# Optimization experiments

Hardware: AMD Instinct MI355X
Metric: run time of the kernel (lower is better)

## Reference

```python
import jax, jax.numpy as jnp
import numpy as np

E, TOPK, H, I = 8, 2, 2048, 5632
T = 4096


def setup_inputs() -> dict:
    key = jax.random.key(0)
    k1, k2, k3, k4 = jax.random.split(key, 4)
    hidden_states = jax.random.normal(k1, (T, H), dtype=jnp.float32)
    gate_w = jax.random.normal(k2, (E, H), dtype=jnp.float32) * (1.0 / np.sqrt(H))
    # fused gate+up projection: [E, 2*I, H]
    w13 = jax.random.normal(k3, (E, 2 * I, H), dtype=jnp.float32) * (1.0 / np.sqrt(H))
    # down projection: [E, H, I]
    w2 = jax.random.normal(k4, (E, H, I), dtype=jnp.float32) * (1.0 / np.sqrt(I))
    return {"hidden_states": hidden_states, "gate_w": gate_w, "w13": w13, "w2": w2, "top_k": TOPK}


def reference(hidden_states, gate_w, w13, w2, top_k):
    num_experts = gate_w.shape[0]
    inter = w2.shape[2]
    # router: fp32 gate logits -> softmax -> top-k -> renormalize (FusedMoE renormalize=True)
    logits = hidden_states.astype(jnp.float32) @ gate_w.T          # [T, E]
    probs = jax.nn.softmax(logits, axis=-1)
    vals, idx = jax.lax.top_k(probs, top_k)                        # [T, k]
    vals = vals / jnp.sum(vals, axis=-1, keepdims=True)
    # dense routing weight matrix [T, E] (zero outside top-k)
    dense_w = jnp.sum(jax.nn.one_hot(idx, num_experts, dtype=vals.dtype) * vals[..., None], axis=1)

    def body(acc, inputs):
        w13_e, w2_e, we = inputs                                   # [2I,H], [H,I], [T]
        gu = hidden_states @ w13_e.T                               # [T, 2I]
        g, u = gu[:, :inter], gu[:, inter:]
        h = jax.nn.silu(g) * u                                     # SwiGLU
        y = h @ w2_e.T                                             # [T, H]
        return acc + we[:, None] * y, None

    acc0 = jnp.zeros_like(hidden_states)
    out, _ = jax.lax.scan(body, acc0, (w13, w2, dense_w.T))
    return out
```

## Files before the change

kernel.cpp:

```cpp
#include <hip/hip_runtime.h>

#define T_TOK 4096
#define H_DIM 2048
#define I_DIM 5632
#define NE 8

typedef _Float16 f16;
typedef _Float16 f16x8 __attribute__((ext_vector_type(8)));
typedef float f32x4 __attribute__((ext_vector_type(4)));

#define OFF_META   0
#define OFF_BTOK   256
#define OFF_BW     (256 + 32768)
#define OFF_RE     (256 + 2 * 32768)
#define OFF_RW     (256 + 3 * 32768)
#define OFF_TP     (256 + 4 * 32768)
#define OFF_HSB    (256 + 5 * 32768)
#define OFF_WF     (OFF_HSB + (size_t)T_TOK * H_DIM * 2)

typedef const __attribute__((address_space(1))) unsigned int guint;
typedef __attribute__((address_space(3))) unsigned int luint;

__device__ __forceinline__ int swzk(int r, int bir) {
    return (bir & 15) | ((((bir >> 4) ^ r) & 7) << 4);
}

__global__ void cvt_w_kernel(const float* __restrict__ src, f16* __restrict__ dst, int n8) {
    int stride = gridDim.x * blockDim.x;
    for (int i = blockIdx.x * blockDim.x + threadIdx.x; i < n8; i += stride) {
        size_t b = (size_t)i * 8;
        float4 a = *(const float4*)(src + b);
        float4 c = *(const float4*)(src + b + 4);
        f16x8 v;
        v[0] = (f16)a.x; v[1] = (f16)a.y; v[2] = (f16)a.z; v[3] = (f16)a.w;
        v[4] = (f16)c.x; v[5] = (f16)c.y; v[6] = (f16)c.z; v[7] = (f16)c.w;
        *(f16x8*)(dst + b) = v;
    }
}

__global__ void prep_kernel(const float* __restrict__ w13, f16* __restrict__ w13f, int n8_w13,
                            int cvt13_b,
                            const float* __restrict__ hs, f16* __restrict__ hsb,
                            const float* __restrict__ gw,
                            int* __restrict__ re, float* __restrict__ rw,
                            int* __restrict__ counts) {
    int id = blockIdx.x;
    if (id < cvt13_b) {
        int stride = cvt13_b * 256;
        for (int i = id * 256 + threadIdx.x; i < n8_w13; i += stride) {
            size_t b = (size_t)i * 8;
            float4 a = *(const float4*)(w13 + b);
            float4 c = *(const float4*)(w13 + b + 4);
            f16x8 v;
            v[0] = (f16)a.x; v[1] = (f16)a.y; v[2] = (f16)a.z; v[3] = (f16)a.w;
            v[4] = (f16)c.x; v[5] = (f16)c.y; v[6] = (f16)c.z; v[7] = (f16)c.w;
            *(f16x8*)(w13f + b) = v;
        }
        return;
    }
    id -= cvt13_b;
    if (id < 1024) {
        const int n8 = T_TOK * H_DIM / 8;
        int stride = 1024 * 256;
        for (int i = id * 256 + threadIdx.x; i < n8; i += stride) {
            size_t b = (size_t)i * 8;
            float4 a = *(const float4*)(hs + b);
            float4 c = *(const float4*)(hs + b + 4);
            f16x8 v;
            v[0] = (f16)a.x; v[1] = (f16)a.y; v[2] = (f16)a.z; v[3] = (f16)a.w;
            v[4] = (f16)c.x; v[5] = (f16)c.y; v[6] = (f16)c.z; v[7] = (f16)c.w;
            *(f16x8*)(hsb + b) = v;
        }
        return;
    }
    id -= 1024;
    int lane = threadIdx.x & 63;
    int t = id * 4 + (threadIdx.x >> 6);
    float acc[NE];
#pragma unroll
    for (int e = 0; e < NE; ++e) acc[e] = 0.f;
    const float* x = hs + (size_t)t * H_DIM;
    for (int i = lane; i < H_DIM; i += 64) {
        float xv = x[i];
#pragma unroll
        for (int e = 0; e < NE; ++e) acc[e] += xv * gw[e * H_DIM + i];
    }
#pragma unroll
    for (int e = 0; e < NE; ++e)
        for (int off = 32; off > 0; off >>= 1) acc[e] += __shfl_xor(acc[e], off);
    if (lane == 0) {
        int i1 = 0; float l1 = acc[0];
#pragma unroll
        for (int e = 1; e < NE; ++e) if (acc[e] > l1) { l1 = acc[e]; i1 = e; }
        int i2 = -1; float l2 = -1e30f;
#pragma unroll
        for (int e = 0; e < NE; ++e) if (e != i1 && acc[e] > l2) { l2 = acc[e]; i2 = e; }
        float aa = __expf(l2 - l1);
        float s = 1.f / (1.f + aa);
        re[t * 2] = i1; re[t * 2 + 1] = i2;
        rw[t * 2] = s;  rw[t * 2 + 1] = aa * s;
        atomicAdd(&counts[i1], 1);
        atomicAdd(&counts[i2], 1);
    }
}

__global__ void scan_kernel(int* __restrict__ meta) {
    if (threadIdx.x == 0) {
        int s = 0;
        for (int e = 0; e < NE; ++e) { meta[8 + e] = s; meta[16 + e] = s; s += meta[e]; }
    }
}

__global__ void place_kernel(const int* __restrict__ re, const float* __restrict__ rw,
                             int* __restrict__ cursor, int* __restrict__ btok,
                             float* __restrict__ bwv, int* __restrict__ tpos) {
    int t = blockIdx.x * 256 + threadIdx.x;
    if (t >= T_TOK) return;
#pragma unroll
    for (int s = 0; s < 2; ++s) {
        int e = re[t * 2 + s];
        int p = atomicAdd(&cursor[e], 1);
        btok[p] = t;
        bwv[p] = rw[t * 2 + s];
        tpos[t * 2 + s] = p;
    }
}

__device__ __forceinline__ void decode_panel(int id, int npx, int e_arg, int e_base,
                                             int& e, int& bx, int& by) {
    if (e_arg >= 0) { e = e_arg; bx = id >> 5; by = id & 31; return; }
    int sg  = id >> 8;
    int rem = id & 255;
    by = rem >> 3;
    int P = sg * 8 + (rem & 7);
    e = e_base + P / npx; bx = P % npx;
}

__global__ __launch_bounds__(256, 4) void gemm1_kernel(
    const f16* __restrict__ w13f, const f16* __restrict__ hsb, f16* __restrict__ hb,
    const int* __restrict__ counts, const int* __restrict__ offs,
    const int* __restrict__ btok,
    const float* __restrict__ cvt_src, f16* __restrict__ cvt_dst, int cvt_n8, int cvt_blocks,
    int e_arg, int e_base, int global_h)
{
    if ((int)blockIdx.x < cvt_blocks) {
        int stride = cvt_blocks * 256;
        for (int i = blockIdx.x * 256 + threadIdx.x; i < cvt_n8; i += stride) {
            size_t b = (size_t)i * 8;
            float4 a = *(const float4*)(cvt_src + b);
            float4 c = *(const float4*)(cvt_src + b + 4);
            f16x8 v;
            v[0] = (f16)a.x; v[1] = (f16)a.y; v[2] = (f16)a.z; v[3] = (f16)a.w;
            v[4] = (f16)c.x; v[5] = (f16)c.y; v[6] = (f16)c.z; v[7] = (f16)c.w;
            *(f16x8*)(cvt_dst + b) = v;
        }
        return;
    }
    int e, bx, by;
    decode_panel((int)blockIdx.x - cvt_blocks, 88, e_arg, e_base, e, bx, by);
    const int n_e = counts[e];
    if (by * 128 >= n_e) return;
    const int boff = offs[e];
    const f16* We = (e_arg >= 0) ? w13f : (w13f + (size_t)e * (2 * I_DIM) * H_DIM);

    const int tid = threadIdx.x;
    const int lane = tid & 63;
    const int wid = tid >> 6;
    const int wm = wid >> 1, wn = wid & 1;
    const int l15 = lane & 15;

    __shared__ f16 As[128 * 64];
    __shared__ f16 Bs[128 * 64];

    const f16* gA[4]; const f16* gB[4]; int dstc[4];
#pragma unroll
    for (int i = 0; i < 4; ++i) {
        int c = i * 256 + tid;
        int r = c >> 3;
        dstc[i] = c * 16;
        int slot = ((c & 7) ^ (r & 7)) * 8;
        int idx = by * 128 + r;
        idx = idx < n_e ? idx : n_e - 1;
        gA[i] = hsb + (size_t)btok[boff + idx] * H_DIM + slot;
        int wrow = (r < 64) ? (bx * 64 + r) : (I_DIM + bx * 64 + (r - 64));
        gB[i] = We + (size_t)wrow * H_DIM + slot;
    }

    f32x4 ag[4][2], au[4][2];
#pragma unroll
    for (int m = 0; m < 4; ++m)
#pragma unroll
        for (int n = 0; n < 2; ++n) { ag[m][n] = (f32x4)0.f; au[m][n] = (f32x4)0.f; }

    const int NT = H_DIM / 64;

#pragma unroll 1
    for (int kt = 0; kt < NT; ++kt) {
        __syncthreads();
        const int k0 = kt * 64;
#pragma unroll
        for (int i = 0; i < 4; ++i) {
            __builtin_amdgcn_global_load_lds((guint*)(gA[i] + k0), (luint*)((char*)As + dstc[i]), 16, 0, 0);
            __builtin_amdgcn_global_load_lds((guint*)(gB[i] + k0), (luint*)((char*)Bs + dstc[i]), 16, 0, 0);
        }
        __syncthreads();
#pragma unroll
        for (int kh = 0; kh < 2; ++kh) {
            const int kb = kh * 64 + (lane >> 4) * 16;
            f16x8 a[4], bg[2], bu[2];
#pragma unroll
            for (int m = 0; m < 4; ++m) {
                int r = wm * 64 + m * 16 + l15;
                a[m] = *(const f16x8*)((const char*)As + r * 128 + swzk(r, kb));
            }
#pragma unroll
            for (int n = 0; n < 2; ++n) {
                int rg = wn * 32 + n * 16 + l15;
                bg[n] = *(const f16x8*)((const char*)Bs + rg * 128 + swzk(rg, kb));
                int ru = 64 + rg;
                bu[n] = *(const f16x8*)((const char*)Bs + ru * 128 + swzk(ru, kb));
            }
#pragma unroll
            for (int m = 0; m < 4; ++m)
#pragma unroll
                for (int n = 0; n < 2; ++n) {
                    ag[m][n] = __builtin_amdgcn_mfma_f32_16x16x32_f16(a[m], bg[n], ag[m][n], 0, 0, 0);
                    au[m][n] = __builtin_amdgcn_mfma_f32_16x16x32_f16(a[m], bu[n], au[m][n], 0, 0, 0);
                }
        }
    }

    const int hbase = (global_h ? boff : 0) + by * 128;
#pragma unroll
    for (int m = 0; m < 4; ++m) {
        int rl0 = wm * 64 + m * 16 + ((lane >> 4) << 2);
#pragma unroll
        for (int r = 0; r < 4; ++r) {
            int rl = rl0 + r;
            if (by * 128 + rl < n_e) {
#pragma unroll
                for (int n = 0; n < 2; ++n) {
                    float g = ag[m][n][r];
                    float u = au[m][n][r];
                    float h = g / (1.f + __expf(-g)) * u;
                    hb[(size_t)(hbase + rl) * I_DIM + bx * 64 + wn * 32 + n * 16 + l15] = (f16)h;
                }
            }
        }
    }
}

__global__ __launch_bounds__(512, 4) void gemm2_kernel(
    const f16* __restrict__ w2f, const f16* __restrict__ hb, float* __restrict__ y,
    const int* __restrict__ counts, const int* __restrict__ offs,
    const int* __restrict__ btok, int e_arg, int global_h)
{
    int e, bx, by;
    decode_panel(blockIdx.x, 8, e_arg, 0, e, bx, by);
    const int n_e = counts[e];
    if (by * 128 >= n_e) return;
    const int boff = offs[e];
    const f16* We = (e_arg >= 0) ? w2f : (w2f + (size_t)e * H_DIM * I_DIM);

    const int tid = threadIdx.x;
    const int lane = tid & 63;
    const int wid = tid >> 6;
    const int wm = wid >> 2;
    const int wn = wid & 3;
    const int l15 = lane & 15;

    __shared__ f16 As[128 * 64];
    __shared__ f16 Bs[256 * 64];

    const int hb0 = global_h ? boff : 0;
    const f16* gA[2]; int dA[2];
#pragma unroll
    for (int i = 0; i < 2; ++i) {
        int c = i * 512 + tid;
        int r = c >> 3;
        dA[i] = c * 16;
        int slot = ((c & 7) ^ (r & 7)) * 8;
        int idx = by * 128 + r;
        idx = idx < n_e ? idx : n_e - 1;
        gA[i] = hb + (size_t)(hb0 + idx) * I_DIM + slot;
    }
    const f16* gB[4]; int dB[4];
#pragma unroll
    for (int j = 0; j < 4; ++j) {
        int c = j * 512 + tid;
        int r = c >> 3;
        dB[j] = c * 16;
        int slot = ((c & 7) ^ (r & 7)) * 8;
        gB[j] = We + (size_t)(bx * 256 + r) * I_DIM + slot;
    }

    f32x4 acc[4][4];
#pragma unroll
    for (int m = 0; m < 4; ++m)
#pragma unroll
        for (int n = 0; n < 4; ++n) acc[m][n] = (f32x4)0.f;

    const int NT = I_DIM / 64;

#pragma unroll 1
    for (int kt = 0; kt < NT; ++kt) {
        __syncthreads();
        const int k0 = kt * 64;
#pragma unroll
        for (int i = 0; i < 2; ++i)
            __builtin_amdgcn_global_load_lds((guint*)(gA[i] + k0), (luint*)((char*)As + dA[i]), 16, 0, 0);
#pragma unroll
        for (int j = 0; j < 4; ++j)
            __builtin_amdgcn_global_load_lds((guint*)(gB[j] + k0), (luint*)((char*)Bs + dB[j]), 16, 0, 0);
        __syncthreads();
#pragma unroll
        for (int kh = 0; kh < 2; ++kh) {
            const int kb = kh * 64 + (lane >> 4) * 16;
            f16x8 a[4], b[4];
#pragma unroll
            for (int m = 0; m < 4; ++m) {
                int r = wm * 64 + m * 16 + l15;
                a[m] = *(const f16x8*)((const char*)As + r * 128 + swzk(r, kb));
            }
#pragma unroll
            for (int n = 0; n < 4; ++n) {
                int r = wn * 64 + n * 16 + l15;
                b[n] = *(const f16x8*)((const char*)Bs + r * 128 + swzk(r, kb));
            }
#pragma unroll
            for (int m = 0; m < 4; ++m)
#pragma unroll
                for (int n = 0; n < 4; ++n)
                    acc[m][n] = __builtin_amdgcn_mfma_f32_16x16x32_f16(a[m], b[n], acc[m][n], 0, 0, 0);
        }
    }

#pragma unroll
    for (int m = 0; m < 4; ++m) {
        int rl0 = wm * 64 + m * 16 + ((lane >> 4) << 2);
#pragma unroll
        for (int r = 0; r < 4; ++r) {
            int rl = rl0 + r;
            if (by * 128 + rl < n_e) {
                int p = boff + by * 128 + rl;
#pragma unroll
                for (int n = 0; n < 4; ++n)
                    y[(size_t)p * H_DIM + bx * 256 + wn * 64 + n * 16 + l15] = acc[m][n][r];
            }
        }
    }
}

__global__ void reduce_kernel(const float* __restrict__ y, const int* __restrict__ tpos,
                              const float* __restrict__ bwv, float* __restrict__ out) {
    int t = blockIdx.x;
    int p0 = tpos[t * 2], p1 = tpos[t * 2 + 1];
    float w0 = bwv[p0], w1 = bwv[p1];
    const float4* y0 = (const float4*)(y + (size_t)p0 * H_DIM);
    const float4* y1 = (const float4*)(y + (size_t)p1 * H_DIM);
    float4* o = (float4*)(out + (size_t)t * H_DIM);
    for (int i = threadIdx.x; i < H_DIM / 4; i += 256) {
        float4 a = y0[i], b = y1[i];
        float4 r;
        r.x = w0 * a.x + w1 * b.x;
        r.y = w0 * a.y + w1 * b.y;
        r.z = w0 * a.z + w1 * b.z;
        r.w = w0 * a.w + w1 * b.w;
        o[i] = r;
    }
}

extern "C" void kernel_launch(void* const* d_in, const int* in_sizes, int n_in,
                              void* d_out, int out_size, void* d_ws, size_t ws_size,
                              hipStream_t stream) {
    const float* hs  = (const float*)d_in[0];
    const float* gw  = (const float*)d_in[1];
    const float* w13 = (const float*)d_in[2];
    const float* w2  = (const float*)d_in[3];
    float* out = (float*)d_out;

    char* ws = (char*)d_ws;
    int*   meta = (int*)(ws + OFF_META);
    int*   btok = (int*)(ws + OFF_BTOK);
    float* bwv  = (float*)(ws + OFF_BW);
    int*   re   = (int*)(ws + OFF_RE);
    float* rw   = (float*)(ws + OFF_RW);
    int*   tpos = (int*)(ws + OFF_TP);
    f16*   hsb  = (f16*)(ws + OFF_HSB);

    hipMemsetAsync(meta, 0, 256, stream);

    const size_t w13_elems = (size_t)NE * 2 * I_DIM * H_DIM;
    const size_t w13_half  = w13_elems / 2;
    const size_t w2_elems  = (size_t)NE * H_DIM * I_DIM;

    size_t o_w13f = OFF_WF;
    size_t o_w2f  = o_w13f + w13_elems * 2;
    size_t o_hb   = o_w2f + w2_elems * 2;
    size_t o_y    = o_hb + (size_t)2 * T_TOK * I_DIM * 2;
    size_t need_full = o_y + (size_t)2 * T_TOK * H_DIM * 4;

    size_t f_w13 = OFF_WF;
    size_t f_w2  = f_w13 + (size_t)2 * I_DIM * H_DIM * 2;
    size_t f_hb  = f_w2 + (size_t)H_DIM * I_DIM * 2;
    size_t f_y   = f_hb + (size_t)T_TOK * I_DIM * 2;

    if (ws_size >= need_full) {
        f16* w13f = (f16*)(ws + o_w13f);
        f16* w2f  = (f16*)(ws + o_w2f);
        f16* hb   = (f16*)(ws + o_hb);
        float* y  = (float*)(ws + o_y);
        prep_kernel<<<3072 + 1024 + 1024, 256, 0, stream>>>(
            w13, w13f, (int)(w13_half / 8), 3072, hs, hsb, gw, re, rw, meta);
        scan_kernel<<<1, 64, 0, stream>>>(meta);
        place_kernel<<<T_TOK / 256, 256, 0, stream>>>(re, rw, meta + 16, btok, bwv, tpos);
        gemm1_kernel<<<2048 + 352 * 32, 256, 0, stream>>>(
            w13f, hsb, hb, meta, meta + 8, btok,
            w13 + w13_half, (f16*)(ws + o_w13f) + w13_half, (int)(w13_half / 8), 2048, -1, 0, 1);
        gemm1_kernel<<<2048 + 352 * 32, 256, 0, stream>>>(
            w13f, hsb, hb, meta, meta + 8, btok,
            w2, w2f, (int)(w2_elems / 8), 2048, -1, 4, 1);
        gemm2_kernel<<<64 * 32, 512, 0, stream>>>(w2f, hb, y, meta, meta + 8, btok, -1, 1);
        reduce_kernel<<<T_TOK, 256, 0, stream>>>(y, tpos, bwv, out);
    } else {
        f16* w13f = (f16*)(ws + f_w13);
        f16* w2f  = (f16*)(ws + f_w2);
        f16* hb   = (f16*)(ws + f_hb);
        float* y  = (float*)(ws + f_y);
        prep_kernel<<<1024 + 1024, 256, 0, stream>>>(
            w13, (f16*)nullptr, 0, 0, hs, hsb, gw, re, rw, meta);
        scan_kernel<<<1, 64, 0, stream>>>(meta);
        place_kernel<<<T_TOK / 256, 256, 0, stream>>>(re, rw, meta + 16, btok, bwv, tpos);
        const size_t w13_slice = (size_t)2 * I_DIM * H_DIM;
        const size_t w2_slice  = (size_t)H_DIM * I_DIM;
        for (int e = 0; e < NE; ++e) {
            cvt_w_kernel<<<2048, 256, 0, stream>>>(w13 + e * w13_slice, w13f, (int)(w13_slice / 8));
            gemm1_kernel<<<2048 + 88 * 32, 256, 0, stream>>>(
                w13f, hsb, hb, meta, meta + 8, btok,
                w2 + e * w2_slice, w2f, (int)(w2_slice / 8), 2048, e, 0, 0);
            gemm2_kernel<<<8 * 32, 512, 0, stream>>>(w2f, hb, y, meta, meta + 8, btok, e, 0);
        }
        reduce_kernel<<<T_TOK, 256, 0, stream>>>(y, tpos, bwv, out);
    }
}
```

Baseline: 1.185 ms.

## Widen gemm1 tiles to 128 intermediate columns and merge the two expert-half launches

```diff
diff --git a/kernel.cpp b/kernel.cpp
--- a/kernel.cpp
+++ b/kernel.cpp
@@ -126,26 +126,26 @@
     }
 }
 
-__device__ __forceinline__ void decode_panel(int id, int npx, int e_arg, int e_base,
+__device__ __forceinline__ void decode_panel(int id, int npx, int e_arg,
                                              int& e, int& bx, int& by) {
     if (e_arg >= 0) { e = e_arg; bx = id >> 5; by = id & 31; return; }
     int sg  = id >> 8;
     int rem = id & 255;
     by = rem >> 3;
     int P = sg * 8 + (rem & 7);
-    e = e_base + P / npx; bx = P % npx;
-}
-
-__global__ __launch_bounds__(256, 4) void gemm1_kernel(
+    e = P / npx; bx = P % npx;
+}
+
+__global__ __launch_bounds__(512, 4) void gemm1_kernel(
     const f16* __restrict__ w13f, const f16* __restrict__ hsb, f16* __restrict__ hb,
     const int* __restrict__ counts, const int* __restrict__ offs,
     const int* __restrict__ btok,
     const float* __restrict__ cvt_src, f16* __restrict__ cvt_dst, int cvt_n8, int cvt_blocks,
-    int e_arg, int e_base, int global_h)
+    int e_arg, int global_h)
 {
     if ((int)blockIdx.x < cvt_blocks) {
-        int stride = cvt_blocks * 256;
-        for (int i = blockIdx.x * 256 + threadIdx.x; i < cvt_n8; i += stride) {
+        int stride = cvt_blocks * 512;
+        for (int i = blockIdx.x * 512 + threadIdx.x; i < cvt_n8; i += stride) {
             size_t b = (size_t)i * 8;
             float4 a = *(const float4*)(cvt_src + b);
             float4 c = *(const float4*)(cvt_src + b + 4);
@@ -157,7 +157,7 @@
         return;
     }
     int e, bx, by;
-    decode_panel((int)blockIdx.x - cvt_blocks, 88, e_arg, e_base, e, bx, by);
+    decode_panel((int)blockIdx.x - cvt_blocks, 44, e_arg, e, bx, by);
     const int n_e = counts[e];
     if (by * 128 >= n_e) return;
     const int boff = offs[e];
@@ -166,24 +166,33 @@
     const int tid = threadIdx.x;
     const int lane = tid & 63;
     const int wid = tid >> 6;
-    const int wm = wid >> 1, wn = wid & 1;
+    const int wm = wid >> 2;
+    const int wn = wid & 3;
     const int l15 = lane & 15;
 
     __shared__ f16 As[128 * 64];
-    __shared__ f16 Bs[128 * 64];
-
-    const f16* gA[4]; const f16* gB[4]; int dstc[4];
-#pragma unroll
-    for (int i = 0; i < 4; ++i) {
-        int c = i * 256 + tid;
+    __shared__ f16 Bs[256 * 64];
+
+    const f16* gA[2]; int dA[2];
+#pragma unroll
+    for (int i = 0; i < 2; ++i) {
+        int c = i * 512 + tid;
         int r = c >> 3;
-        dstc[i] = c * 16;
+        dA[i] = c * 16;
         int slot = ((c & 7) ^ (r & 7)) * 8;
         int idx = by * 128 + r;
         idx = idx < n_e ? idx : n_e - 1;
         gA[i] = hsb + (size_t)btok[boff + idx] * H_DIM + slot;
-        int wrow = (r < 64) ? (bx * 64 + r) : (I_DIM + bx * 64 + (r - 64));
-        gB[i] = We + (size_t)wrow * H_DIM + slot;
+    }
+    const f16* gB[4]; int dB[4];
+#pragma unroll
+    for (int j = 0; j < 4; ++j) {
+        int c = j * 512 + tid;
+        int r = c >> 3;
+        dB[j] = c * 16;
+        int slot = ((c & 7) ^ (r & 7)) * 8;
+        int wrow = (r < 128) ? (bx * 128 + r) : (I_DIM + bx * 128 + (r - 128));
+        gB[j] = We + (size_t)wrow * H_DIM + slot;
     }
 
     f32x4 ag[4][2], au[4][2];
@@ -199,10 +208,11 @@
         __syncthreads();
         const int k0 = kt * 64;
 #pragma unroll
-        for (int i = 0; i < 4; ++i) {
-            __builtin_amdgcn_global_load_lds((guint*)(gA[i] + k0), (luint*)((char*)As + dstc[i]), 16, 0, 0);
-            __builtin_amdgcn_global_load_lds((guint*)(gB[i] + k0), (luint*)((char*)Bs + dstc[i]), 16, 0, 0);
-        }
+        for (int i = 0; i < 2; ++i)
+            __builtin_amdgcn_global_load_lds((guint*)(gA[i] + k0), (luint*)((char*)As + dA[i]), 16, 0, 0);
+#pragma unroll
+        for (int j = 0; j < 4; ++j)
+            __builtin_amdgcn_global_load_lds((guint*)(gB[j] + k0), (luint*)((char*)Bs + dB[j]), 16, 0, 0);
         __syncthreads();
 #pragma unroll
         for (int kh = 0; kh < 2; ++kh) {
@@ -217,7 +227,7 @@
             for (int n = 0; n < 2; ++n) {
                 int rg = wn * 32 + n * 16 + l15;
                 bg[n] = *(const f16x8*)((const char*)Bs + rg * 128 + swzk(rg, kb));
-                int ru = 64 + rg;
+                int ru = 128 + rg;
                 bu[n] = *(const f16x8*)((const char*)Bs + ru * 128 + swzk(ru, kb));
             }
 #pragma unroll
@@ -243,7 +253,7 @@
                     float g = ag[m][n][r];
                     float u = au[m][n][r];
                     float h = g / (1.f + __expf(-g)) * u;
-                    hb[(size_t)(hbase + rl) * I_DIM + bx * 64 + wn * 32 + n * 16 + l15] = (f16)h;
+                    hb[(size_t)(hbase + rl) * I_DIM + bx * 128 + wn * 32 + n * 16 + l15] = (f16)h;
                 }
             }
         }
@@ -256,7 +266,7 @@
     const int* __restrict__ btok, int e_arg, int global_h)
 {
     int e, bx, by;
-    decode_panel(blockIdx.x, 8, e_arg, 0, e, bx, by);
+    decode_panel(blockIdx.x, 8, e_arg, e, bx, by);
     const int n_e = counts[e];
     if (by * 128 >= n_e) return;
     const int boff = offs[e];
@@ -391,7 +401,6 @@
     hipMemsetAsync(meta, 0, 256, stream);
 
     const size_t w13_elems = (size_t)NE * 2 * I_DIM * H_DIM;
-    const size_t w13_half  = w13_elems / 2;
     const size_t w2_elems  = (size_t)NE * H_DIM * I_DIM;
 
     size_t o_w13f = OFF_WF;
@@ -411,15 +420,12 @@
         f16* hb   = (f16*)(ws + o_hb);
         float* y  = (float*)(ws + o_y);
         prep_kernel<<<3072 + 1024 + 1024, 256, 0, stream>>>(
-            w13, w13f, (int)(w13_half / 8), 3072, hs, hsb, gw, re, rw, meta);
+            w13, w13f, (int)(w13_elems / 8), 3072, hs, hsb, gw, re, rw, meta);
         scan_kernel<<<1, 64, 0, stream>>>(meta);
         place_kernel<<<T_TOK / 256, 256, 0, stream>>>(re, rw, meta + 16, btok, bwv, tpos);
-        gemm1_kernel<<<2048 + 352 * 32, 256, 0, stream>>>(
+        gemm1_kernel<<<1024 + 352 * 32, 512, 0, stream>>>(
             w13f, hsb, hb, meta, meta + 8, btok,
-            w13 + w13_half, (f16*)(ws + o_w13f) + w13_half, (int)(w13_half / 8), 2048, -1, 0, 1);
-        gemm1_kernel<<<2048 + 352 * 32, 256, 0, stream>>>(
-            w13f, hsb, hb, meta, meta + 8, btok,
-            w2, w2f, (int)(w2_elems / 8), 2048, -1, 4, 1);
+            w2, w2f, (int)(w2_elems / 8), 1024, -1, 1);
         gemm2_kernel<<<64 * 32, 512, 0, stream>>>(w2f, hb, y, meta, meta + 8, btok, -1, 1);
         reduce_kernel<<<T_TOK, 256, 0, stream>>>(y, tpos, bwv, out);
     } else {
@@ -435,9 +441,9 @@
         const size_t w2_slice  = (size_t)H_DIM * I_DIM;
         for (int e = 0; e < NE; ++e) {
             cvt_w_kernel<<<2048, 256, 0, stream>>>(w13 + e * w13_slice, w13f, (int)(w13_slice / 8));
-            gemm1_kernel<<<2048 + 88 * 32, 256, 0, stream>>>(
+            gemm1_kernel<<<1024 + 44 * 32, 512, 0, stream>>>(
                 w13f, hsb, hb, meta, meta + 8, btok,
-                w2 + e * w2_slice, w2f, (int)(w2_slice / 8), 2048, e, 0, 0);
+                w2 + e * w2_slice, w2f, (int)(w2_slice / 8), 1024, e, 0);
             gemm2_kernel<<<8 * 32, 512, 0, stream>>>(w2f, hb, y, meta, meta + 8, btok, e, 0);
         }
         reduce_kernel<<<T_TOK, 256, 0, stream>>>(y, tpos, bwv, out);
```

Measured after the change: 1.191 ms. About the same (+0.5%).
